# Optimization experiments

Hardware: AMD Instinct MI355X
Metric: run time of the kernel (lower is better)

The kernel has to match this reference:

```python
import jax, jax.numpy as jnp
import numpy as np

DIM = 2560
N_HEAD = 32
HEAD_DIM = 80
ROT_DIM = 32  # head_dim * partial_rotary_factor
INTER = 10240
EPS = 1e-5
BASE = 10000.0


def setup_inputs() -> dict:
    key = jax.random.key(0)
    ks = jax.random.split(key, 12)
    B, S, D, I = 1, 2048, DIM, INTER
    s = lambda k, shape, scale: (jax.random.normal(k, shape, jnp.float32) * scale)
    return {
        "x": s(ks[0], (B, S, D), 1.0),
        "input_pos": jnp.arange(S, dtype=jnp.int32),
        "mask": jnp.tril(jnp.ones((S, S), dtype=bool)),
        "ln_w": jnp.ones((D,), jnp.float32),
        "ln_b": jnp.zeros((D,), jnp.float32),
        "wqkv_w": s(ks[1], (3 * D, D), 0.02),
        "wqkv_b": jnp.zeros((3 * D,), jnp.float32),
        "wo_w": s(ks[2], (D, D), 0.02),
        "wo_b": jnp.zeros((D,), jnp.float32),
        "w1_w": s(ks[3], (I, D), 0.02),
        "w1_b": jnp.zeros((I,), jnp.float32),
        "w2_w": s(ks[4], (D, I), 0.02),
        "w2_b": jnp.zeros((D,), jnp.float32),
    }


def _rope_cos_sin(positions):
    # positions: [S] int; returns cos,sin of shape [S, ROT_DIM]
    inv_freq = 1.0 / (BASE ** (jnp.arange(0, ROT_DIM, 2, dtype=jnp.float32) / ROT_DIM))
    freqs = positions.astype(jnp.float32)[:, None] * inv_freq[None, :]  # [S, ROT/2]
    emb = jnp.concatenate([freqs, freqs], axis=-1)  # [S, ROT]
    return jnp.cos(emb), jnp.sin(emb)


def _rotate_half(t):
    t1, t2 = jnp.split(t, 2, axis=-1)
    return jnp.concatenate([-t2, t1], axis=-1)


def _apply_rope(t, cos, sin):
    # t: [B,H,S,hd]; rotary applied to first ROT_DIM dims (partial rotary)
    t_rot, t_pass = t[..., :ROT_DIM], t[..., ROT_DIM:]
    t_rot = t_rot * cos[None, None] + _rotate_half(t_rot) * sin[None, None]
    return jnp.concatenate([t_rot, t_pass], axis=-1)


def reference(x, input_pos, mask, ln_w, ln_b, wqkv_w, wqkv_b, wo_w, wo_b,
              w1_w, w1_b, w2_w, w2_b):
    B, S, D = x.shape
    H, hd = N_HEAD, HEAD_DIM
    # shared LayerNorm (parallel block)
    mu = jnp.mean(x, axis=-1, keepdims=True)
    var = jnp.mean(jnp.square(x - mu), axis=-1, keepdims=True)
    h = (x - mu) * jax.lax.rsqrt(var + EPS) * ln_w + ln_b

    # fused QKV
    qkv = h @ wqkv_w.T + wqkv_b  # [B,S,3D]
    q, k, v = jnp.split(qkv, 3, axis=-1)
    q = q.reshape(B, S, H, hd).transpose(0, 2, 1, 3)  # [B,H,S,hd]
    k = k.reshape(B, S, H, hd).transpose(0, 2, 1, 3)
    v = v.reshape(B, S, H, hd).transpose(0, 2, 1, 3)

    cos, sin = _rope_cos_sin(input_pos)
    q = _apply_rope(q, cos, sin)
    k = _apply_rope(k, cos, sin)

    # causal attention
    scores = jnp.einsum("bhqd,bhkd->bhqk", q, k) / np.sqrt(hd).astype(np.float32)
    scores = jnp.where(mask[None, None], scores, jnp.float32(-1e9))
    attn = jax.nn.softmax(scores, axis=-1)
    y = jnp.einsum("bhqk,bhkd->bhqd", attn, v)  # [B,H,S,hd]
    y = y.transpose(0, 2, 1, 3).reshape(B, S, D)
    attn_out = y @ wo_w.T + wo_b

    # fused MLP (phi2: gelu_new / tanh approx)
    ffn = jax.nn.gelu(h @ w1_w.T + w1_b, approximate=True) @ w2_w.T + w2_b

    return attn_out + ffn + x
```

## Files before the change

kernel.cpp:

```cpp
#include <hip/hip_runtime.h>
#include <cstdint>

#define S_LEN 2048
#define DMODEL 2560
#define NHEADS 32
#define HDIM 80
#define DINTER 10240

typedef unsigned short u16;
typedef __bf16 bf16x8 __attribute__((ext_vector_type(8)));
typedef float f32x4 __attribute__((ext_vector_type(4)));

__device__ __forceinline__ float us2f(u16 u) {
  return __builtin_bit_cast(float, ((uint32_t)u) << 16);
}
__device__ __forceinline__ u16 f2us(float f) {
  uint32_t x = __builtin_bit_cast(uint32_t, f);
  x += 0x7fffu + ((x >> 16) & 1u);
  return (u16)(x >> 16);
}

typedef __attribute__((address_space(1))) void gas_void;
typedef __attribute__((address_space(3))) void las_void;
__device__ __forceinline__ void gld16(const void* g, void* l) {
  __builtin_amdgcn_global_load_lds((gas_void*)g, (las_void*)l, 16, 0, 0);
}

__global__ void f2b_kernel(const float* __restrict__ src, u16* __restrict__ dst) {
  const size_t i = ((size_t)blockIdx.x * 256 + threadIdx.x) * 8;
  const float4 a = *(const float4*)(src + i);
  const float4 b = *(const float4*)(src + i + 4);
  u16 o[8] = {f2us(a.x), f2us(a.y), f2us(a.z), f2us(a.w),
              f2us(b.x), f2us(b.y), f2us(b.z), f2us(b.w)};
  *(uint4*)(dst + i) = *(uint4*)o;
}

__global__ void ln_kernel(const float* __restrict__ x, const float* __restrict__ w,
                          const float* __restrict__ b, u16* __restrict__ h) {
  const int s = blockIdx.x, tid = threadIdx.x;
  const float* xr = x + (size_t)s * DMODEL;
  float v[10];
  float sum = 0.f, sq = 0.f;
#pragma unroll
  for (int j = 0; j < 10; j++) {
    v[j] = xr[tid + j * 256];
    sum += v[j];
    sq += v[j] * v[j];
  }
#pragma unroll
  for (int o = 32; o > 0; o >>= 1) {
    sum += __shfl_down(sum, o, 64);
    sq += __shfl_down(sq, o, 64);
  }
  __shared__ float red[8];
  const int wave = tid >> 6, lane = tid & 63;
  if (lane == 0) { red[wave] = sum; red[4 + wave] = sq; }
  __syncthreads();
  sum = red[0] + red[1] + red[2] + red[3];
  sq = red[4] + red[5] + red[6] + red[7];
  const float mu = sum * (1.0f / DMODEL);
  const float var = sq * (1.0f / DMODEL) - mu * mu;
  const float rstd = rsqrtf(var + 1e-5f);
  u16* hr = h + (size_t)s * DMODEL;
#pragma unroll
  for (int j = 0; j < 10; j++) {
    const int d = tid + j * 256;
    hr[d] = f2us((v[j] - mu) * rstd * w[d] + b[d]);
  }
}

template <int ACT, int OUTF32>
__global__ void gemm_bt(const u16* __restrict__ A, const u16* __restrict__ B,
                        const float* __restrict__ bias, void* __restrict__ Cv,
                        int M, int N, int K) {
  __shared__ __align__(16) u16 As[128 * 32];
  __shared__ __align__(16) u16 Bs[128 * 32];
  const int tid = threadIdx.x;
  const int wave = tid >> 6, lane = tid & 63;
  const int quad = lane >> 4, l15 = lane & 15;
  const int wm = wave >> 1, wn = wave & 1;
  const int bm = blockIdx.y, bn = blockIdx.x;

  const int srow = lane >> 2;
  const int scol = (lane & 3) * 8;
  const size_t aBase = (size_t)(bm * 128 + wave * 32 + srow) * K + scol;
  const size_t aBase2 = aBase + (size_t)16 * K;
  const size_t bBase = (size_t)(bn * 128 + wave * 32 + srow) * K + scol;
  const size_t bBase2 = bBase + (size_t)16 * K;
  u16* AsW0 = As + (wave * 32) * 32;
  u16* AsW1 = As + (wave * 32 + 16) * 32;
  u16* BsW0 = Bs + (wave * 32) * 32;
  u16* BsW1 = Bs + (wave * 32 + 16) * 32;

  f32x4 acc[4][4] = {};

  for (int k0 = 0; k0 < K; k0 += 32) {
    gld16(A + aBase + k0, AsW0);
    gld16(A + aBase2 + k0, AsW1);
    gld16(B + bBase + k0, BsW0);
    gld16(B + bBase2 + k0, BsW1);
    __syncthreads();
    bf16x8 af[4], bf[4];
#pragma unroll
    for (int mt = 0; mt < 4; mt++)
      af[mt] = *(const bf16x8*)&As[(wm * 64 + mt * 16 + l15) * 32 + quad * 8];
#pragma unroll
    for (int nt = 0; nt < 4; nt++)
      bf[nt] = *(const bf16x8*)&Bs[(wn * 64 + nt * 16 + l15) * 32 + quad * 8];
#pragma unroll
    for (int mt = 0; mt < 4; mt++)
#pragma unroll
      for (int nt = 0; nt < 4; nt++)
        acc[mt][nt] =
            __builtin_amdgcn_mfma_f32_16x16x32_bf16(af[mt], bf[nt], acc[mt][nt], 0, 0, 0);
    __syncthreads();
  }

#pragma unroll
  for (int nt = 0; nt < 4; nt++) {
    const int col = bn * 128 + wn * 64 + nt * 16 + l15;
    const float bv = bias[col];
#pragma unroll
    for (int mt = 0; mt < 4; mt++) {
      const int row0 = bm * 128 + wm * 64 + mt * 16 + quad * 4;
#pragma unroll
      for (int r = 0; r < 4; r++) {
        float v = acc[mt][nt][r] + bv;
        if (ACT == 1) {
          const float t = v * (0.7978845608f + 0.0356774081f * v * v);
          v = 0.5f * v * (1.0f + tanhf(t));
        }
        if (OUTF32)
          ((float*)Cv)[(size_t)(row0 + r) * N + col] = v;
        else
          ((u16*)Cv)[(size_t)(row0 + r) * N + col] = f2us(v);
      }
    }
  }
}

__global__ void rope_kernel(u16* __restrict__ qkv, const int* __restrict__ pos) {
  const int idx = blockIdx.x * 256 + threadIdx.x;
  const int i = idx & 15;
  const int which = (idx >> 4) & 1;
  const int hh = (idx >> 5) & 31;
  const int s = idx >> 10;
  const float p = (float)pos[s];
  const float freq = p * expf(-0.57564627324851f * (float)i);
  float sn, c;
  sincosf(freq, &sn, &c);
  u16* base = qkv + (size_t)s * (3 * DMODEL) + which * DMODEL + hh * HDIM + i;
  const float t0 = us2f(base[0]), t1 = us2f(base[16]);
  base[0] = f2us(t0 * c - t1 * sn);
  base[16] = f2us(t1 * c + t0 * sn);
}

__global__ void attn_kernel(const u16* __restrict__ qkv, u16* __restrict__ y) {
  const int qt = (int)gridDim.x - 1 - (int)blockIdx.x;
  const int h = blockIdx.y;
  const int tid = threadIdx.x, wave = tid >> 6, lane = tid & 63;
  const int quad = lane >> 4, l15 = lane & 15;
  const int qbase = qt * 64;

  __shared__ __align__(16) u16 Qs[64 * 96];
  __shared__ __align__(16) u16 Ks[32 * 96];
  __shared__ __align__(16) u16 Vts[80 * 40];
  __shared__ __align__(16) u16 Ps[4][16 * 40];

  for (int i = tid; i < 64 * 96; i += 256) Qs[i] = 0;
  for (int i = tid; i < 32 * 96; i += 256) Ks[i] = 0;
  __syncthreads();

  {
    const int r = tid >> 2, c = tid & 3;
    const u16* src = qkv + (size_t)(qbase + r) * (3 * DMODEL) + h * HDIM + c * 20;
    u16* dst = Qs + r * 96 + c * 20;
#pragma unroll
    for (int j = 0; j < 5; j++) {
      ushort4 uv = *(const ushort4*)(src + j * 4);
      ushort4 ov;
      ov.x = f2us(us2f(uv.x) * 0.11180339887f);
      ov.y = f2us(us2f(uv.y) * 0.11180339887f);
      ov.z = f2us(us2f(uv.z) * 0.11180339887f);
      ov.w = f2us(us2f(uv.w) * 0.11180339887f);
      *(ushort4*)(dst + j * 4) = ov;
    }
  }

  float m_i[4], l_i[4];
  f32x4 oacc[5] = {};
#pragma unroll
  for (int r = 0; r < 4; r++) { m_i[r] = -1e30f; l_i[r] = 0.f; }

  const int n_iter = qt * 2 + 2;
  __syncthreads();

  for (int it = 0; it < n_iter; ++it) {
    const int kc0 = it * 32;
    if (tid < 128) {
      const int r = tid >> 2, c = tid & 3;
      const u16* src =
          qkv + (size_t)(kc0 + r) * (3 * DMODEL) + DMODEL + h * HDIM + c * 20;
      u16* dst = Ks + r * 96 + c * 20;
#pragma unroll
      for (int j = 0; j < 5; j++)
        *(ushort4*)(dst + j * 4) = *(const ushort4*)(src + j * 4);
    } else {
      const int u = tid - 128;
      const int r = u >> 2, c = u & 3;
      const u16* src =
          qkv + (size_t)(kc0 + r) * (3 * DMODEL) + 2 * DMODEL + h * HDIM + c * 20;
#pragma unroll
      for (int j = 0; j < 5; j++) {
        ushort4 vv = *(const ushort4*)(src + j * 4);
        const int d0 = c * 20 + j * 4;
        Vts[(d0 + 0) * 40 + r] = vv.x;
        Vts[(d0 + 1) * 40 + r] = vv.y;
        Vts[(d0 + 2) * 40 + r] = vv.z;
        Vts[(d0 + 3) * 40 + r] = vv.w;
      }
    }
    __syncthreads();

    f32x4 st[2] = {};
#pragma unroll
    for (int ks = 0; ks < 3; ks++) {
      bf16x8 aq = *(const bf16x8*)&Qs[(wave * 16 + l15) * 96 + ks * 32 + quad * 8];
#pragma unroll
      for (int t = 0; t < 2; t++) {
        bf16x8 bk = *(const bf16x8*)&Ks[(t * 16 + l15) * 96 + ks * 32 + quad * 8];
        st[t] = __builtin_amdgcn_mfma_f32_16x16x32_bf16(aq, bk, st[t], 0, 0, 0);
      }
    }

    float sv[2][4], mx[4];
#pragma unroll
    for (int r = 0; r < 4; r++) {
      const int qr = qbase + wave * 16 + quad * 4 + r;
#pragma unroll
      for (int t = 0; t < 2; t++) {
        const int kc = kc0 + t * 16 + l15;
        sv[t][r] = (kc <= qr) ? st[t][r] : -1e30f;
      }
      mx[r] = fmaxf(sv[0][r], sv[1][r]);
    }
#pragma unroll
    for (int o = 1; o < 16; o <<= 1)
#pragma unroll
      for (int r = 0; r < 4; r++) mx[r] = fmaxf(mx[r], __shfl_xor(mx[r], o, 64));

    float alpha[4], rs[4];
#pragma unroll
    for (int r = 0; r < 4; r++) {
      const float mnew = fmaxf(m_i[r], mx[r]);
      alpha[r] = __expf(m_i[r] - mnew);
      m_i[r] = mnew;
      const float p0 = __expf(sv[0][r] - mnew);
      const float p1 = __expf(sv[1][r] - mnew);
      rs[r] = p0 + p1;
      Ps[wave][(quad * 4 + r) * 40 + l15] = f2us(p0);
      Ps[wave][(quad * 4 + r) * 40 + 16 + l15] = f2us(p1);
    }
#pragma unroll
    for (int o = 1; o < 16; o <<= 1)
#pragma unroll
      for (int r = 0; r < 4; r++) rs[r] += __shfl_xor(rs[r], o, 64);
#pragma unroll
    for (int r = 0; r < 4; r++) l_i[r] = l_i[r] * alpha[r] + rs[r];
#pragma unroll
    for (int dt = 0; dt < 5; dt++)
#pragma unroll
      for (int r = 0; r < 4; r++) oacc[dt][r] *= alpha[r];

    bf16x8 pf = *(const bf16x8*)&Ps[wave][l15 * 40 + quad * 8];
#pragma unroll
    for (int dt = 0; dt < 5; dt++) {
      bf16x8 vf = *(const bf16x8*)&Vts[(dt * 16 + l15) * 40 + quad * 8];
      oacc[dt] = __builtin_amdgcn_mfma_f32_16x16x32_bf16(pf, vf, oacc[dt], 0, 0, 0);
    }
    __syncthreads();
  }

#pragma unroll
  for (int dt = 0; dt < 5; dt++)
#pragma unroll
    for (int r = 0; r < 4; r++) {
      const int row = qbase + wave * 16 + quad * 4 + r;
      y[(size_t)row * DMODEL + h * HDIM + dt * 16 + l15] = f2us(oacc[dt][r] / l_i[r]);
    }
}

__global__ void add3_kernel(const float* __restrict__ x, const float* __restrict__ a,
                            const float* __restrict__ f, float* __restrict__ out) {
  const size_t idx = ((size_t)blockIdx.x * 256 + threadIdx.x) * 4;
  const float4 vx = *(const float4*)(x + idx);
  const float4 va = *(const float4*)(a + idx);
  const float4 vf = *(const float4*)(f + idx);
  float4 vo;
  vo.x = vx.x + va.x + vf.x;
  vo.y = vx.y + va.y + vf.y;
  vo.z = vx.z + va.z + vf.z;
  vo.w = vx.w + va.w + vf.w;
  *(float4*)(out + idx) = vo;
}

extern "C" void kernel_launch(void* const* d_in, const int* in_sizes, int n_in,
                              void* d_out, int out_size, void* d_ws, size_t ws_size,
                              hipStream_t stream) {
  const float* x = (const float*)d_in[0];
  const int* pos = (const int*)d_in[1];
  const float* ln_w = (const float*)d_in[3];
  const float* ln_b = (const float*)d_in[4];
  const float* wqkv_w = (const float*)d_in[5];
  const float* wqkv_b = (const float*)d_in[6];
  const float* wo_w = (const float*)d_in[7];
  const float* wo_b = (const float*)d_in[8];
  const float* w1_w = (const float*)d_in[9];
  const float* w1_b = (const float*)d_in[10];
  const float* w2_w = (const float*)d_in[11];
  const float* w2_b = (const float*)d_in[12];
  float* out = (float*)d_out;

  char* ws = (char*)d_ws;
  u16* wbuf = (u16*)(ws);
  float* attn = (float*)(ws + 16777216);
  u16* h = (u16*)(ws + 52428800);
  u16* ffn1 = (u16*)(ws + 62914560);
  u16* qkv = (u16*)(ws + 62914560);
  u16* yAtt = (u16*)(ws + 94371840);
  float* ffn2 = (float*)(ws + 104857600);

  ln_kernel<<<S_LEN, 256, 0, stream>>>(x, ln_w, ln_b, h);

  f2b_kernel<<<(DINTER * DMODEL) / 2048, 256, 0, stream>>>(w1_w, wbuf);
  gemm_bt<1, 0><<<dim3(DINTER / 128, S_LEN / 128), 256, 0, stream>>>(
      h, wbuf, w1_b, ffn1, S_LEN, DINTER, DMODEL);
  f2b_kernel<<<(DMODEL * DINTER) / 2048, 256, 0, stream>>>(w2_w, wbuf);
  gemm_bt<0, 1><<<dim3(DMODEL / 128, S_LEN / 128), 256, 0, stream>>>(
      ffn1, wbuf, w2_b, ffn2, S_LEN, DMODEL, DINTER);

  f2b_kernel<<<(3 * DMODEL * DMODEL) / 2048, 256, 0, stream>>>(wqkv_w, wbuf);
  gemm_bt<0, 0><<<dim3(3 * DMODEL / 128, S_LEN / 128), 256, 0, stream>>>(
      h, wbuf, wqkv_b, qkv, S_LEN, 3 * DMODEL, DMODEL);
  rope_kernel<<<(S_LEN * NHEADS * 2 * 16) / 256, 256, 0, stream>>>(qkv, pos);
  attn_kernel<<<dim3(S_LEN / 64, NHEADS), 256, 0, stream>>>(qkv, yAtt);
  f2b_kernel<<<(DMODEL * DMODEL) / 2048, 256, 0, stream>>>(wo_w, wbuf);
  gemm_bt<0, 1><<<dim3(DMODEL / 128, S_LEN / 128), 256, 0, stream>>>(
      yAtt, wbuf, wo_b, attn, S_LEN, DMODEL, DMODEL);

  add3_kernel<<<(S_LEN * DMODEL / 4) / 256, 256, 0, stream>>>(x, attn, ffn2, out);
}
```

Before: 1.075 ms.

## Split-K the down-projection GEMMs with atomic accumulation into output and swizzle tiles

The W2 and Wo GEMMs now split K across gridDim.z (4 and 2 slices) and atomically add fp32 partials straight into the output. The output is pre-initialised with x plus both biases, which removes the separate add3 pass and the fp32 intermediate buffers. The split-K is meant to lift the small 320-tile grids so they fill the GPU. A block-index swizzle groups tiles into 4-column by 16-row bands for better L2 reuse of A and B. The cost is atomic traffic and a floating-point summation order that is no longer deterministic.

Result: faster. 1.031 ms (-4.2%).

```diff
diff --git a/kernel.cpp b/kernel.cpp
--- a/kernel.cpp
+++ b/kernel.cpp
@@ -33,6 +33,23 @@
   u16 o[8] = {f2us(a.x), f2us(a.y), f2us(a.z), f2us(a.w),
               f2us(b.x), f2us(b.y), f2us(b.z), f2us(b.w)};
   *(uint4*)(dst + i) = *(uint4*)o;
+}
+
+__global__ void initout_kernel(const float* __restrict__ x,
+                               const float* __restrict__ wo_b,
+                               const float* __restrict__ w2_b,
+                               float* __restrict__ out) {
+  const size_t idx = ((size_t)blockIdx.x * 256 + threadIdx.x) * 4;
+  const int c0 = (int)(idx % DMODEL);
+  const float4 vx = *(const float4*)(x + idx);
+  const float4 b1 = *(const float4*)(wo_b + c0);
+  const float4 b2 = *(const float4*)(w2_b + c0);
+  float4 vo;
+  vo.x = vx.x + b1.x + b2.x;
+  vo.y = vx.y + b1.y + b2.y;
+  vo.z = vx.z + b1.z + b2.z;
+  vo.w = vx.w + b1.w + b2.w;
+  *(float4*)(out + idx) = vo;
 }
 
 __global__ void ln_kernel(const float* __restrict__ x, const float* __restrict__ w,
@@ -69,7 +86,7 @@
   }
 }
 
-template <int ACT, int OUTF32>
+template <int ACT, int MODE>
 __global__ void gemm_bt(const u16* __restrict__ A, const u16* __restrict__ B,
                         const float* __restrict__ bias, void* __restrict__ Cv,
                         int M, int N, int K) {
@@ -79,7 +96,14 @@
   const int wave = tid >> 6, lane = tid & 63;
   const int quad = lane >> 4, l15 = lane & 15;
   const int wm = wave >> 1, wn = wave & 1;
-  const int bm = blockIdx.y, bn = blockIdx.x;
+
+  const int flat = blockIdx.x + gridDim.x * blockIdx.y;
+  const int r_ = flat & 63;
+  const int bn = (flat >> 6) * 4 + (r_ & 3);
+  const int bm = r_ >> 2;
+
+  const int Kc = K / gridDim.z;
+  const int kbeg = blockIdx.z * Kc;
 
   const int srow = lane >> 2;
   const int scol = (lane & 3) * 8;
@@ -94,7 +118,7 @@
 
   f32x4 acc[4][4] = {};
 
-  for (int k0 = 0; k0 < K; k0 += 32) {
+  for (int k0 = kbeg; k0 < kbeg + Kc; k0 += 32) {
     gld16(A + aBase + k0, AsW0);
     gld16(A + aBase2 + k0, AsW1);
     gld16(B + bBase + k0, BsW0);
@@ -119,7 +143,7 @@
 #pragma unroll
   for (int nt = 0; nt < 4; nt++) {
     const int col = bn * 128 + wn * 64 + nt * 16 + l15;
-    const float bv = bias[col];
+    const float bv = (MODE == 0) ? bias[col] : 0.f;
 #pragma unroll
     for (int mt = 0; mt < 4; mt++) {
       const int row0 = bm * 128 + wm * 64 + mt * 16 + quad * 4;
@@ -130,10 +154,10 @@
           const float t = v * (0.7978845608f + 0.0356774081f * v * v);
           v = 0.5f * v * (1.0f + tanhf(t));
         }
-        if (OUTF32)
-          ((float*)Cv)[(size_t)(row0 + r) * N + col] = v;
+        if (MODE == 0)
+          ((u16*)Cv)[(size_t)(row0 + r) * N + col] = f2us(v);
         else
-          ((u16*)Cv)[(size_t)(row0 + r) * N + col] = f2us(v);
+          atomicAdd((float*)Cv + (size_t)(row0 + r) * N + col, v);
       }
     }
   }
@@ -288,20 +312,6 @@
       const int row = qbase + wave * 16 + quad * 4 + r;
       y[(size_t)row * DMODEL + h * HDIM + dt * 16 + l15] = f2us(oacc[dt][r] / l_i[r]);
     }
-}
-
-__global__ void add3_kernel(const float* __restrict__ x, const float* __restrict__ a,
-                            const float* __restrict__ f, float* __restrict__ out) {
-  const size_t idx = ((size_t)blockIdx.x * 256 + threadIdx.x) * 4;
-  const float4 vx = *(const float4*)(x + idx);
-  const float4 va = *(const float4*)(a + idx);
-  const float4 vf = *(const float4*)(f + idx);
-  float4 vo;
-  vo.x = vx.x + va.x + vf.x;
-  vo.y = vx.y + va.y + vf.y;
-  vo.z = vx.z + va.z + vf.z;
-  vo.w = vx.w + va.w + vf.w;
-  *(float4*)(out + idx) = vo;
 }
 
 extern "C" void kernel_launch(void* const* d_in, const int* in_sizes, int n_in,
@@ -323,30 +333,27 @@
 
   char* ws = (char*)d_ws;
   u16* wbuf = (u16*)(ws);
-  float* attn = (float*)(ws + 16777216);
   u16* h = (u16*)(ws + 52428800);
   u16* ffn1 = (u16*)(ws + 62914560);
   u16* qkv = (u16*)(ws + 62914560);
   u16* yAtt = (u16*)(ws + 94371840);
-  float* ffn2 = (float*)(ws + 104857600);
 
   ln_kernel<<<S_LEN, 256, 0, stream>>>(x, ln_w, ln_b, h);
+  initout_kernel<<<(S_LEN * DMODEL / 4) / 256, 256, 0, stream>>>(x, wo_b, w2_b, out);
 
   f2b_kernel<<<(DINTER * DMODEL) / 2048, 256, 0, stream>>>(w1_w, wbuf);
-  gemm_bt<1, 0><<<dim3(DINTER / 128, S_LEN / 128), 256, 0, stream>>>(
+  gemm_bt<1, 0><<<dim3(DINTER / 128, S_LEN / 128, 1), 256, 0, stream>>>(
       h, wbuf, w1_b, ffn1, S_LEN, DINTER, DMODEL);
   f2b_kernel<<<(DMODEL * DINTER) / 2048, 256, 0, stream>>>(w2_w, wbuf);
-  gemm_bt<0, 1><<<dim3(DMODEL / 128, S_LEN / 128), 256, 0, stream>>>(
-      ffn1, wbuf, w2_b, ffn2, S_LEN, DMODEL, DINTER);
+  gemm_bt<0, 2><<<dim3(DMODEL / 128, S_LEN / 128, 4), 256, 0, stream>>>(
+      ffn1, wbuf, w2_b, out, S_LEN, DMODEL, DINTER);
 
   f2b_kernel<<<(3 * DMODEL * DMODEL) / 2048, 256, 0, stream>>>(wqkv_w, wbuf);
-  gemm_bt<0, 0><<<dim3(3 * DMODEL / 128, S_LEN / 128), 256, 0, stream>>>(
+  gemm_bt<0, 0><<<dim3(3 * DMODEL / 128, S_LEN / 128, 1), 256, 0, stream>>>(
       h, wbuf, wqkv_b, qkv, S_LEN, 3 * DMODEL, DMODEL);
   rope_kernel<<<(S_LEN * NHEADS * 2 * 16) / 256, 256, 0, stream>>>(qkv, pos);
   attn_kernel<<<dim3(S_LEN / 64, NHEADS), 256, 0, stream>>>(qkv, yAtt);
   f2b_kernel<<<(DMODEL * DMODEL) / 2048, 256, 0, stream>>>(wo_w, wbuf);
-  gemm_bt<0, 1><<<dim3(DMODEL / 128, S_LEN / 128), 256, 0, stream>>>(
-      yAtt, wbuf, wo_b, attn, S_LEN, DMODEL, DMODEL);
-
-  add3_kernel<<<(S_LEN * DMODEL / 4) / 256, 256, 0, stream>>>(x, attn, ffn2, out);
-}
+  gemm_bt<0, 2><<<dim3(DMODEL / 128, S_LEN / 128, 2), 256, 0, stream>>>(
+      yAtt, wbuf, wo_b, out, S_LEN, DMODEL, DMODEL);
+}
```
